# Optimization experiments

Measured on AMD Instinct MI355X. Metric: run time of the kernel, lower is better.

## Reference

```python
import jax, jax.numpy as jnp
import numpy as np


def setup_inputs() -> dict:
    key = jax.random.key(0)
    ks = jax.random.split(key, 5)
    B, T, H, L = 32, 1024, 512, 2
    scale = 1.0 / np.sqrt(H)
    x = jax.random.normal(ks[0], (B, T, H), dtype=jnp.float32)
    Wi = jax.random.normal(ks[1], (L, 4 * H, H), dtype=jnp.float32) * scale
    bi = jax.random.normal(ks[2], (L, 4 * H), dtype=jnp.float32) * scale
    Ws = jax.random.normal(ks[3], (L, 4 * H, H), dtype=jnp.float32) * scale
    # state_linearity bias: zeros except forget slice [H:2H] = 1 (reset_parameters)
    bs = jnp.zeros((L, 4 * H), dtype=jnp.float32)
    bs = bs.at[:, H:2 * H].set(1.0)
    return {"x": x, "Wi": Wi, "bi": bi, "Ws": Ws, "bs": bs}


def reference(x, Wi, bi, Ws, bs):
    # x: [B,T,H]; Wi/Ws: [L,4C,H]; bi/bs: [L,4C]; here C == H (no projection layer)
    B, T, H = x.shape
    L = Wi.shape[0]
    C = H

    def step(carry, x_t):
        h, c = carry  # each [L,B,C]
        inp = x_t  # [B,H]
        new_h, new_c = [], []
        for j in range(L):
            z = inp @ Wi[j].T + bi[j] + h[j] @ Ws[j].T + bs[j]  # [B,4C]
            ig = jax.nn.sigmoid(z[:, 0 * C:1 * C])
            fg = jax.nn.sigmoid(z[:, 1 * C:2 * C])
            gg = jnp.tanh(z[:, 2 * C:3 * C])
            og = jax.nn.sigmoid(z[:, 3 * C:4 * C])
            c_j = ig * gg + fg * c[j]
            h_j = og * jnp.tanh(c_j) + inp  # residual skip connection
            inp = h_j
            new_h.append(h_j)
            new_c.append(c_j)
        return (jnp.stack(new_h), jnp.stack(new_c)), inp

    h0 = jnp.zeros((L, B, C), dtype=x.dtype)
    c0 = jnp.zeros((L, B, C), dtype=x.dtype)
    (h_f, c_f), ys = jax.lax.scan(step, (h0, c0), jnp.swapaxes(x, 0, 1))
    out = jnp.swapaxes(ys, 0, 1)  # [B,T,H]
    # final states as (B, L, H) matching module layout
    return out, jnp.swapaxes(h_f, 0, 1), jnp.swapaxes(c_f, 0, 1)
```

## Files before the change

kernel.cpp:

```cpp
#include <hip/hip_runtime.h>


typedef unsigned int uint32;
typedef unsigned short ushort;

constexpr int B = 32, T = 1024, H = 512, NL = 2;
constexpr int KTOT = 2 * H;
constexpr int BH   = B * H;
constexpr size_t BTH = (size_t)B * T * H;
constexpr size_t BLH = (size_t)B * NL * H;

using bf16x8  = __attribute__((ext_vector_type(8))) short;
using floatx4 = __attribute__((ext_vector_type(4))) float;
using uint4v  = __attribute__((ext_vector_type(4))) uint32;

__device__ __forceinline__ float frcp(float x) { return __builtin_amdgcn_rcpf(x); }
__device__ __forceinline__ float sigm(float v) { return frcp(1.0f + __expf(-v)); }
__device__ __forceinline__ float tanh_fast(float v) {
    return 1.0f - 2.0f * frcp(1.0f + __expf(2.0f * v));
}

__device__ __forceinline__ ushort f2bf(float f) {
    uint32 u = __builtin_bit_cast(uint32, f);
    u += 0x7fffu + ((u >> 16) & 1u);
    return (ushort)(u >> 16);
}

__launch_bounds__(512, 1)
__global__ void lstm_persist(const float* __restrict__ x,
                             const float* __restrict__ Wi,
                             const float* __restrict__ bi,
                             const float* __restrict__ Ws,
                             const float* __restrict__ bs,
                             float* __restrict__ out,
                             uint32* __restrict__ ctrl,
                             uint32* __restrict__ h0pk,
                             uint32* __restrict__ h1pk)
{
    extern __shared__ short smem[];
    short* whi = smem;
    short* wlo = smem + 32 * KTOT;
    float* red = (float*)(smem + 64 * KTOT);

    const int wg    = blockIdx.x;
    const int tid   = threadIdx.x;
    const int layer = wg & 1;
    const int rg    = wg >> 1;
    const int chb   = rg * 8;

    for (int i = tid; i < 32 * KTOT; i += 512) {
        const int n = i >> 10, k = i & (KTOT - 1);
        const int g = n >> 3, c = n & 7;
        const int grow = g * H + chb + c;
        const float v = (k < H) ? Wi[((size_t)layer * 4 * H + grow) * H + k]
                                : Ws[((size_t)layer * 4 * H + grow) * H + (k - H)];
        const ushort hb = f2bf(v);
        const float  hf = __builtin_bit_cast(float, (uint32)hb << 16);
        const ushort lb = f2bf(v - hf);
        const int off = (n * 128 + ((k >> 3) ^ n)) * 8 + (k & 7);
        whi[off] = (short)hb;
        wlo[off] = (short)lb;
    }

    const int lane = tid & 63;
    const int w    = tid >> 6;
    const int mt   = w & 1;
    const int kq   = w >> 1;
    const int quad = lane >> 4;
    const int mrow = lane & 15;
    const int bb   = mt * 16 + mrow;
    const int nn   = mrow;

    const int ec = tid & 7, eb = tid >> 3;
    float cs = 0.f;
    float bias_[4] = {0.f, 0.f, 0.f, 0.f};
    if (tid < 256) {
        #pragma unroll
        for (int g = 0; g < 4; ++g) {
            const int grow = g * H + chb + ec;
            bias_[g] = bi[layer * 4 * H + grow] + bs[layer * 4 * H + grow];
        }
    }
    __syncthreads();

    for (int s = 0; s <= T; ++s) {
        const int t = (layer == 0) ? s : s - 1;
        const bool active = (t >= 0 && t < T);

        float resid = 0.f;
        if (active && tid < 256) {
            const int ch = chb + ec;
            if (layer == 0) {
                resid = x[((size_t)eb * T + t) * H + ch];
            } else {
                const uint32 rp = __hip_atomic_load(
                    &h0pk[(size_t)(t & 1) * BH + (size_t)eb * H + ch],
                    __ATOMIC_RELAXED, __HIP_MEMORY_SCOPE_AGENT);
                resid = __builtin_bit_cast(float, rp << 16)
                      + __builtin_bit_cast(float, rp & 0xffff0000u);
            }
        }

        if (active) {
            floatx4 acc0 = {0.f, 0.f, 0.f, 0.f};
            floatx4 acc1 = {0.f, 0.f, 0.f, 0.f};
            floatx4 acc2 = {0.f, 0.f, 0.f, 0.f};
            floatx4 acc3 = {0.f, 0.f, 0.f, 0.f};

            if (layer == 0 && kq < 2) {
                const float* xb = x + ((size_t)bb * T + t) * H + kq * 256 + quad * 8;
                #pragma unroll
                for (int st = 0; st < 8; ++st) {
                    const float4* p = (const float4*)(xb + st * 32);
                    const float4 f0 = p[0], f1 = p[1];
                    const float vv[8] = {f0.x, f0.y, f0.z, f0.w, f1.x, f1.y, f1.z, f1.w};
                    bf16x8 ahi, alo;
                    #pragma unroll
                    for (int j = 0; j < 8; ++j) {
                        const ushort hb = f2bf(vv[j]);
                        const float  hf = __builtin_bit_cast(float, (uint32)hb << 16);
                        ahi[j] = (short)hb;
                        alo[j] = (short)f2bf(vv[j] - hf);
                    }
                    const int cb = kq * 32 + st * 4 + quad;
                    const int n1 = 16 + nn;
                    const int woff0 = (nn * 128 + (cb ^ nn)) * 8;
                    const int woff1 = (n1 * 128 + (cb ^ n1)) * 8;
                    const bf16x8 bh0 = *(const bf16x8*)(whi + woff0);
                    const bf16x8 bl0 = *(const bf16x8*)(wlo + woff0);
                    const bf16x8 bh1 = *(const bf16x8*)(whi + woff1);
                    const bf16x8 bl1 = *(const bf16x8*)(wlo + woff1);
                    acc0 = __builtin_amdgcn_mfma_f32_16x16x32_bf16(ahi, bh0, acc0, 0, 0, 0);
                    acc1 = __builtin_amdgcn_mfma_f32_16x16x32_bf16(alo, bh0, acc1, 0, 0, 0);
                    acc1 = __builtin_amdgcn_mfma_f32_16x16x32_bf16(ahi, bl0, acc1, 0, 0, 0);
                    acc2 = __builtin_amdgcn_mfma_f32_16x16x32_bf16(ahi, bh1, acc2, 0, 0, 0);
                    acc3 = __builtin_amdgcn_mfma_f32_16x16x32_bf16(alo, bh1, acc3, 0, 0, 0);
                    acc3 = __builtin_amdgcn_mfma_f32_16x16x32_bf16(ahi, bl1, acc3, 0, 0, 0);
                }
            } else {
                int par, koff;
                const uint32* hbuf;
                if (layer == 0)   { par = (t - 1) & 1; koff = kq * 256 - 512; hbuf = h0pk; }
                else if (kq < 2)  { par = t & 1;       koff = kq * 256;       hbuf = h0pk; }
                else              { par = (t - 1) & 1; koff = kq * 256 - 512; hbuf = h1pk; }
                const uint32* hp = hbuf + (size_t)par * BH + (size_t)bb * H + koff + quad * 8;

                uint4v q0,q1,q2,q3,q4,q5,q6,q7,q8,q9,q10,q11,q12,q13,q14,q15;
                asm volatile(
                    "global_load_dwordx4 %0,  %16, off sc0 sc1\n\t"
                    "global_load_dwordx4 %1,  %16, off offset:16 sc0 sc1\n\t"
                    "global_load_dwordx4 %2,  %16, off offset:128 sc0 sc1\n\t"
                    "global_load_dwordx4 %3,  %16, off offset:144 sc0 sc1\n\t"
                    "global_load_dwordx4 %4,  %16, off offset:256 sc0 sc1\n\t"
                    "global_load_dwordx4 %5,  %16, off offset:272 sc0 sc1\n\t"
                    "global_load_dwordx4 %6,  %16, off offset:384 sc0 sc1\n\t"
                    "global_load_dwordx4 %7,  %16, off offset:400 sc0 sc1\n\t"
                    "global_load_dwordx4 %8,  %16, off offset:512 sc0 sc1\n\t"
                    "global_load_dwordx4 %9,  %16, off offset:528 sc0 sc1\n\t"
                    "global_load_dwordx4 %10, %16, off offset:640 sc0 sc1\n\t"
                    "global_load_dwordx4 %11, %16, off offset:656 sc0 sc1\n\t"
                    "global_load_dwordx4 %12, %16, off offset:768 sc0 sc1\n\t"
                    "global_load_dwordx4 %13, %16, off offset:784 sc0 sc1\n\t"
                    "global_load_dwordx4 %14, %16, off offset:896 sc0 sc1\n\t"
                    "global_load_dwordx4 %15, %16, off offset:912 sc0 sc1\n\t"
                    "s_waitcnt vmcnt(0)"
                    : "=&v"(q0), "=&v"(q1), "=&v"(q2), "=&v"(q3),
                      "=&v"(q4), "=&v"(q5), "=&v"(q6), "=&v"(q7),
                      "=&v"(q8), "=&v"(q9), "=&v"(q10), "=&v"(q11),
                      "=&v"(q12), "=&v"(q13), "=&v"(q14), "=&v"(q15)
                    : "v"(hp)
                    : "memory");
                const uint4v qq[16] = {q0,q1,q2,q3,q4,q5,q6,q7,q8,q9,q10,q11,q12,q13,q14,q15};

                #pragma unroll
                for (int st = 0; st < 8; ++st) {
                    const uint4v ea = qq[2 * st], eb4 = qq[2 * st + 1];
                    uint4v hiw, low;
                    hiw[0] = __builtin_amdgcn_perm(ea[1],  ea[0],  0x05040100u);
                    hiw[1] = __builtin_amdgcn_perm(ea[3],  ea[2],  0x05040100u);
                    hiw[2] = __builtin_amdgcn_perm(eb4[1], eb4[0], 0x05040100u);
                    hiw[3] = __builtin_amdgcn_perm(eb4[3], eb4[2], 0x05040100u);
                    low[0] = __builtin_amdgcn_perm(ea[1],  ea[0],  0x07060302u);
                    low[1] = __builtin_amdgcn_perm(ea[3],  ea[2],  0x07060302u);
                    low[2] = __builtin_amdgcn_perm(eb4[1], eb4[0], 0x07060302u);
                    low[3] = __builtin_amdgcn_perm(eb4[3], eb4[2], 0x07060302u);
                    const bf16x8 ahi = __builtin_bit_cast(bf16x8, hiw);
                    const bf16x8 alo = __builtin_bit_cast(bf16x8, low);
                    const int cb = kq * 32 + st * 4 + quad;
                    const int n1 = 16 + nn;
                    const int woff0 = (nn * 128 + (cb ^ nn)) * 8;
                    const int woff1 = (n1 * 128 + (cb ^ n1)) * 8;
                    const bf16x8 bh0 = *(const bf16x8*)(whi + woff0);
                    const bf16x8 bl0 = *(const bf16x8*)(wlo + woff0);
                    const bf16x8 bh1 = *(const bf16x8*)(whi + woff1);
                    const bf16x8 bl1 = *(const bf16x8*)(wlo + woff1);
                    acc0 = __builtin_amdgcn_mfma_f32_16x16x32_bf16(ahi, bh0, acc0, 0, 0, 0);
                    acc1 = __builtin_amdgcn_mfma_f32_16x16x32_bf16(alo, bh0, acc1, 0, 0, 0);
                    acc1 = __builtin_amdgcn_mfma_f32_16x16x32_bf16(ahi, bl0, acc1, 0, 0, 0);
                    acc2 = __builtin_amdgcn_mfma_f32_16x16x32_bf16(ahi, bh1, acc2, 0, 0, 0);
                    acc3 = __builtin_amdgcn_mfma_f32_16x16x32_bf16(alo, bh1, acc3, 0, 0, 0);
                    acc3 = __builtin_amdgcn_mfma_f32_16x16x32_bf16(ahi, bl1, acc3, 0, 0, 0);
                }
            }
            floatx4 zr0, zr1;
            zr0[0] = acc0[0] + acc1[0]; zr0[1] = acc0[1] + acc1[1];
            zr0[2] = acc0[2] + acc1[2]; zr0[3] = acc0[3] + acc1[3];
            zr1[0] = acc2[0] + acc3[0]; zr1[1] = acc2[1] + acc3[1];
            zr1[2] = acc2[2] + acc3[2]; zr1[3] = acc2[3] + acc3[3];
            *(floatx4*)&red[((w * 2 + 0) * 64 + lane) * 4] = zr0;
            *(floatx4*)&red[((w * 2 + 1) * 64 + lane) * 4] = zr1;
        }
        __syncthreads();

        if (active && tid < 256) {
            const int m = eb & 15, emt = eb >> 4, q = m >> 2, r = m & 3;
            const int ch = chb + ec;
            float z[4];
            #pragma unroll
            for (int g = 0; g < 4; ++g) {
                const int n = g * 8 + ec;
                const int nt = n >> 4, col = n & 15;
                const int li = q * 16 + col;
                float a = bias_[g];
                #pragma unroll
                for (int kqe = 0; kqe < 4; ++kqe)
                    a += red[((((kqe * 2 + emt) * 2) + nt) * 64 + li) * 4 + r];
                z[g] = a;
            }
            const float ig = sigm(z[0]), fg = sigm(z[1]);
            const float gg = tanh_fast(z[2]), og = sigm(z[3]);
            cs = ig * gg + fg * cs;
            const float hn = og * tanh_fast(cs) + resid;

            const size_t hidx = (size_t)(t & 1) * BH + (size_t)eb * H + ch;
            const ushort hb = f2bf(hn);
            const float  hf = __builtin_bit_cast(float, (uint32)hb << 16);
            const ushort lb = f2bf(hn - hf);
            const uint32 pk = (uint32)hb | ((uint32)lb << 16);
            if (layer == 0) {
                __hip_atomic_store(&h0pk[hidx], pk, __ATOMIC_RELAXED, __HIP_MEMORY_SCOPE_AGENT);
            } else {
                __hip_atomic_store(&h1pk[hidx], pk, __ATOMIC_RELAXED, __HIP_MEMORY_SCOPE_AGENT);
                out[((size_t)eb * T + t) * H + ch] = hn;
            }
            if (t == T - 1) {
                out[BTH + ((size_t)eb * NL + layer) * H + ch] = hn;
                out[BTH + BLH + ((size_t)eb * NL + layer) * H + ch] = cs;
            }
        }

        __syncthreads();
        if (s < T) {
            const uint32 epoch = (uint32)s + 1u;
            if (tid < 64) {
                if (tid == 0) {
                    uint32* gcnt = ctrl + (wg >> 3) * 32;
                    const uint32 rr = __hip_atomic_fetch_add(gcnt, 1u, __ATOMIC_RELAXED,
                                                             __HIP_MEMORY_SCOPE_AGENT);
                    if (rr == epoch * 8u - 1u)
                        __hip_atomic_store(&ctrl[512 + (wg >> 3)], epoch,
                                           __ATOMIC_RELAXED, __HIP_MEMORY_SCOPE_AGENT);
                }
                const uint32* fp = ctrl + 512 + (tid & 15);
                for (;;) {
                    uint32 f;
                    asm volatile("global_load_dword %0, %1, off sc0 sc1\n\t"
                                 "s_waitcnt vmcnt(0)"
                                 : "=v"(f) : "v"(fp) : "memory");
                    if (__all(f >= epoch)) break;
                    __builtin_amdgcn_s_sleep(1);
                }
            }
            __syncthreads();
        }
    }
}

extern "C" void kernel_launch(void* const* d_in, const int* in_sizes, int n_in,
                              void* d_out, int out_size, void* d_ws, size_t ws_size,
                              hipStream_t stream) {
    const float* x  = (const float*)d_in[0];
    const float* Wi = (const float*)d_in[1];
    const float* bi = (const float*)d_in[2];
    const float* Ws = (const float*)d_in[3];
    const float* bs = (const float*)d_in[4];
    float* out = (float*)d_out;

    char* wsb = (char*)d_ws;
    uint32* ctrl = (uint32*)wsb;
    uint32* h0pk = (uint32*)(wsb + 4096);
    uint32* h1pk = (uint32*)(wsb + 4096 + 131072);
    const size_t zero_bytes = 4096 + 2 * 131072;

    static const size_t lds_bytes = (size_t)(64 * KTOT) * sizeof(short)
                                  + (size_t)8 * 2 * 64 * 4 * sizeof(float);
    hipFuncSetAttribute((const void*)lstm_persist,
                        hipFuncAttributeMaxDynamicSharedMemorySize, (int)lds_bytes);

    hipMemsetAsync(d_ws, 0, zero_bytes, stream);
    hipLaunchKernelGGL(lstm_persist, dim3(128), dim3(512), lds_bytes, stream,
                       x, Wi, bi, Ws, bs, out, ctrl, h0pk, h1pk);
}
```

Measured before the change: 7.907 ms.

## Replace grid barrier with per-workgroup flags and decouple layers via 4-deep h0 ring

Drops the two-level atomic counter barrier. Each workgroup now publishes its own step flag, and waiters poll every flag directly. Layer-0 workgroups only need layer-1 to be within two steps, so the h0 buffer grows to four slots to let layer 0 run ahead. The next step's x tile is also prefetched into registers before the wait, hiding its load latency. This adds register pressure and 64-flag polling traffic, and relies on the relaxed ordering assumptions holding for the deeper ring.

```diff
diff --git a/kernel.cpp b/kernel.cpp
--- a/kernel.cpp
+++ b/kernel.cpp
@@ -81,6 +81,17 @@
             bias_[g] = bi[layer * 4 * H + grow] + bs[layer * 4 * H + grow];
         }
     }
+
+    const bool xwave = (layer == 0) && (kq < 2);
+    float4 xq[16];
+    if (xwave) {
+        const float* xb = x + ((size_t)bb * T + 0) * H + kq * 256 + quad * 8;
+        #pragma unroll
+        for (int st = 0; st < 8; ++st) {
+            xq[2 * st]     = *(const float4*)(xb + st * 32);
+            xq[2 * st + 1] = *(const float4*)(xb + st * 32 + 4);
+        }
+    }
     __syncthreads();
 
     for (int s = 0; s <= T; ++s) {
@@ -94,7 +105,7 @@
                 resid = x[((size_t)eb * T + t) * H + ch];
             } else {
                 const uint32 rp = __hip_atomic_load(
-                    &h0pk[(size_t)(t & 1) * BH + (size_t)eb * H + ch],
+                    &h0pk[(size_t)(t & 3) * BH + (size_t)eb * H + ch],
                     __ATOMIC_RELAXED, __HIP_MEMORY_SCOPE_AGENT);
                 resid = __builtin_bit_cast(float, rp << 16)
                       + __builtin_bit_cast(float, rp & 0xffff0000u);
@@ -107,12 +118,10 @@
             floatx4 acc2 = {0.f, 0.f, 0.f, 0.f};
             floatx4 acc3 = {0.f, 0.f, 0.f, 0.f};
 
-            if (layer == 0 && kq < 2) {
-                const float* xb = x + ((size_t)bb * T + t) * H + kq * 256 + quad * 8;
+            if (xwave) {
                 #pragma unroll
                 for (int st = 0; st < 8; ++st) {
-                    const float4* p = (const float4*)(xb + st * 32);
-                    const float4 f0 = p[0], f1 = p[1];
+                    const float4 f0 = xq[2 * st], f1 = xq[2 * st + 1];
                     const float vv[8] = {f0.x, f0.y, f0.z, f0.w, f1.x, f1.y, f1.z, f1.w};
                     bf16x8 ahi, alo;
                     #pragma unroll
@@ -140,8 +149,8 @@
             } else {
                 int par, koff;
                 const uint32* hbuf;
-                if (layer == 0)   { par = (t - 1) & 1; koff = kq * 256 - 512; hbuf = h0pk; }
-                else if (kq < 2)  { par = t & 1;       koff = kq * 256;       hbuf = h0pk; }
+                if (layer == 0)   { par = (t - 1) & 3; koff = kq * 256 - 512; hbuf = h0pk; }
+                else if (kq < 2)  { par = t & 3;       koff = kq * 256;       hbuf = h0pk; }
                 else              { par = (t - 1) & 1; koff = kq * 256 - 512; hbuf = h1pk; }
                 const uint32* hp = hbuf + (size_t)par * BH + (size_t)bb * H + koff + quad * 8;
 
@@ -232,14 +241,15 @@
             cs = ig * gg + fg * cs;
             const float hn = og * tanh_fast(cs) + resid;
 
-            const size_t hidx = (size_t)(t & 1) * BH + (size_t)eb * H + ch;
             const ushort hb = f2bf(hn);
             const float  hf = __builtin_bit_cast(float, (uint32)hb << 16);
             const ushort lb = f2bf(hn - hf);
             const uint32 pk = (uint32)hb | ((uint32)lb << 16);
             if (layer == 0) {
+                const size_t hidx = (size_t)(t & 3) * BH + (size_t)eb * H + ch;
                 __hip_atomic_store(&h0pk[hidx], pk, __ATOMIC_RELAXED, __HIP_MEMORY_SCOPE_AGENT);
             } else {
+                const size_t hidx = (size_t)(t & 1) * BH + (size_t)eb * H + ch;
                 __hip_atomic_store(&h1pk[hidx], pk, __ATOMIC_RELAXED, __HIP_MEMORY_SCOPE_AGENT);
                 out[((size_t)eb * T + t) * H + ch] = hn;
             }
@@ -251,23 +261,33 @@
 
         __syncthreads();
         if (s < T) {
-            const uint32 epoch = (uint32)s + 1u;
+            if (xwave && (s + 1) < T) {
+                const float* xb = x + ((size_t)bb * T + (s + 1)) * H + kq * 256 + quad * 8;
+                #pragma unroll
+                for (int st = 0; st < 8; ++st) {
+                    xq[2 * st]     = *(const float4*)(xb + st * 32);
+                    xq[2 * st + 1] = *(const float4*)(xb + st * 32 + 4);
+                }
+            }
+            const uint32 e = (uint32)s + 1u;
+            if (tid == 0)
+                __hip_atomic_store(&ctrl[layer * 64 + rg], e,
+                                   __ATOMIC_RELAXED, __HIP_MEMORY_SCOPE_AGENT);
             if (tid < 64) {
-                if (tid == 0) {
-                    uint32* gcnt = ctrl + (wg >> 3) * 32;
-                    const uint32 rr = __hip_atomic_fetch_add(gcnt, 1u, __ATOMIC_RELAXED,
-                                                             __HIP_MEMORY_SCOPE_AGENT);
-                    if (rr == epoch * 8u - 1u)
-                        __hip_atomic_store(&ctrl[512 + (wg >> 3)], epoch,
-                                           __ATOMIC_RELAXED, __HIP_MEMORY_SCOPE_AGENT);
-                }
-                const uint32* fp = ctrl + 512 + (tid & 15);
+                const uint32* pa = ctrl + tid;
+                const uint32* pb = ctrl + 64 + tid;
                 for (;;) {
-                    uint32 f;
-                    asm volatile("global_load_dword %0, %1, off sc0 sc1\n\t"
+                    uint32 a, b;
+                    asm volatile("global_load_dword %0, %2, off sc0 sc1\n\t"
+                                 "global_load_dword %1, %3, off sc0 sc1\n\t"
                                  "s_waitcnt vmcnt(0)"
-                                 : "=v"(f) : "v"(fp) : "memory");
-                    if (__all(f >= epoch)) break;
+                                 : "=&v"(a), "=&v"(b)
+                                 : "v"(pa), "v"(pb)
+                                 : "memory");
+                    const bool ok = (layer == 0)
+                        ? ((a >= e) && ((int)b >= (int)e - 2))
+                        : ((a >= e) && (b >= e));
+                    if (__all(ok)) break;
                     __builtin_amdgcn_s_sleep(1);
                 }
             }
@@ -289,8 +309,8 @@
     char* wsb = (char*)d_ws;
     uint32* ctrl = (uint32*)wsb;
     uint32* h0pk = (uint32*)(wsb + 4096);
-    uint32* h1pk = (uint32*)(wsb + 4096 + 131072);
-    const size_t zero_bytes = 4096 + 2 * 131072;
+    uint32* h1pk = (uint32*)(wsb + 4096 + 262144);
+    const size_t zero_bytes = 4096 + 262144 + 131072;
 
     static const size_t lds_bytes = (size_t)(64 * KTOT) * sizeof(short)
                                   + (size_t)8 * 2 * 64 * 4 * sizeof(float);
```

Result: slower. 8.872 ms (+12.2%).
